# Kernel optimization log

Measured on AMD Instinct MI355X. Metric: run time of the kernel, lower is better.

Reference implementation:

```python
import jax, jax.numpy as jnp
import numpy as np


def setup_inputs() -> dict:
    key = jax.random.key(0)
    D, H, T, B = 512, 512, 500, 128
    ks = jax.random.split(key, 12)
    tn = lambda k, shape: 0.01 * jax.random.truncated_normal(k, -2.0, 2.0, shape, dtype=jnp.float32)
    return {
        "inputs": jax.random.normal(ks[0], (B, D), dtype=jnp.float32),
        "Wz": tn(ks[1], (D, H)),
        "Wr": tn(ks[2], (D, H)),
        "Wh": tn(ks[3], (D, H)),
        "Uz": tn(ks[4], (H, H)),
        "Ur": tn(ks[5], (H, H)),
        "Uh": tn(ks[6], (H, H)),
        "bz": tn(ks[7], (H,)),
        "br": tn(ks[8], (H,)),
        "bh": tn(ks[9], (H,)),
        "Wo": tn(ks[10], (H, D)),
        "bo": tn(ks[11], (D,)),
        "T": T,
    }


def reference(inputs, Wz, Wr, Wh, Uz, Ur, Uh, bz, br, bh, Wo, bo, T):
    B, D = inputs.shape
    H = Wz.shape[1]

    def step(carry, _):
        h, x = carry  # h: [B,H], x: [B,D]
        r = jax.nn.sigmoid(x @ Wr + h @ Ur + br)
        h_prop = jnp.tanh(x @ Wh + (r * h) @ Uh + bh)
        z = jax.nn.sigmoid(x @ Wz + h @ Uz + bz)
        h_new = jnp.clip((1.0 - z) * h + z * h_prop, -5.0, 5.0)
        out = h_new @ Wo + bo
        return (h_new, out), out

    h0 = jnp.zeros((B, H), dtype=inputs.dtype)
    _, outs = jax.lax.scan(step, (h0, inputs), None, length=T - 1)  # [T-1,B,D]
    full = jnp.concatenate([inputs[None], outs], axis=0)  # [T,B,D]
    return jnp.transpose(full, (1, 0, 2))  # [B,T,D]
```

## Files before the change

### kernel.cpp

```cpp
#include <hip/hip_runtime.h>
#include <cstdint>

#define NB 128
#define DH 512
#define ROWS 528

#define OFF_M   0u
#define OFF_M1  1048576u
#define OFF_UH  2097152u
#define OFF_H   2359296u
#define OFF_RH  2426880u
#define OFF_XT  2494464u
#define OFF_GZ  2562048u
#define OFF_GH  2627584u
#define OFF_CV  2693120u
#define OFF_C1  2695168u
#define OFF_BAR 2697216u

__device__ __forceinline__ float sigm(float x) { return 1.f / (1.f + __expf(-x)); }
__device__ __forceinline__ float tanh_fast(float x) {
  float e = __expf(2.f * fminf(x, 40.f));
  return (e - 1.f) / (e + 1.f);
}

__device__ __forceinline__ float cload(const float* p) {
  return __hip_atomic_load(p, __ATOMIC_RELAXED, __HIP_MEMORY_SCOPE_AGENT);
}
__device__ __forceinline__ void cstore(float* p, float v) {
  __hip_atomic_store(p, v, __ATOMIC_RELAXED, __HIP_MEMORY_SCOPE_AGENT);
}

__global__ __launch_bounds__(256) void gru_pre(
    const float* __restrict__ inputs,
    const float* __restrict__ Wz, const float* __restrict__ Wr, const float* __restrict__ Wh,
    const float* __restrict__ Uz, const float* __restrict__ Ur, const float* __restrict__ Uh,
    const float* __restrict__ bz, const float* __restrict__ br, const float* __restrict__ bh,
    const float* __restrict__ Wo, const float* __restrict__ bo,
    float* __restrict__ ws)
{
  __shared__ float sh[8960];
  const int bid = blockIdx.x, t = threadIdx.x;
  float* Mw  = ws + OFF_M;
  float* M1w = ws + OFF_M1;
  float* Uhw = ws + OFF_UH;
  float* hw  = ws + OFF_H;
  float* rhw = ws + OFF_RH;
  float* xT  = ws + OFF_XT;
  float* cv  = ws + OFF_CV;
  float* c1  = ws + OFF_C1;
  uint32_t* bar = (uint32_t*)(ws + OFF_BAR);

  if (bid < 256) {
    const int kh = bid >> 7, cch = bid & 127;
    const int reg = cch >> 5;
    const int k0 = kh * 256, c0 = cch * 16;
    if (reg == 3) {
      const int cc0 = c0 - 1536;
      for (int i = 0; i < 16; ++i) {
        int idx = t + i * 256;
        int kk = k0 + (idx >> 4), ci = idx & 15;
        Mw[(cch * 512 + kk) * 16 + ci] = Wo[kk * 512 + cc0 + ci];
      }
    } else {
      const float* Ws = (reg == 0) ? Wr : (reg == 1) ? Wz : Wh;
      const float* Us = (reg == 0) ? Ur : (reg == 1) ? Uz : nullptr;
      const int cc0 = c0 - reg * 512;
      const int kl = t;
      const int k = k0 + kl;
      float acc[16];
      #pragma unroll
      for (int c = 0; c < 16; ++c) acc[c] = 0.f;
      for (int jt = 0; jt < 16; ++jt) {
        __syncthreads();
        for (int i = 0; i < 32; ++i) {
          int idx = t + i * 256;
          int kk = idx >> 5, jj = idx & 31;
          sh[kk * 35 + jj] = Wo[(k0 + kk) * 512 + jt * 32 + jj];
        }
        __syncthreads();
        for (int j = 0; j < 32; ++j) {
          float wv = sh[kl * 35 + j];
          const float* wrow = Ws + (jt * 32 + j) * 512 + cc0;
          #pragma unroll
          for (int c = 0; c < 16; ++c) acc[c] = fmaf(wv, wrow[c], acc[c]);
        }
      }
      #pragma unroll
      for (int c = 0; c < 16; ++c) {
        float v = acc[c];
        if (Us) v += Us[k * 512 + cc0 + c];
        Mw[(cch * 512 + k) * 16 + c] = v;
      }
    }
  }
  else if (bid < 264) {
    const int q = bid - 256;
    const int r2 = q >> 1;
    const float* Ws = (r2 == 0) ? Wr : (r2 == 1) ? Wz : (r2 == 2) ? Wh : nullptr;
    const float* bs = (r2 == 0) ? br : (r2 == 1) ? bz : (r2 == 2) ? bh : nullptr;
    for (int round = 0; round < 8; ++round) {
      int col32 = t >> 3, strip = t & 7;
      int c = q * 256 + round * 32 + col32;
      int cc = c & 511;
      float p = 0.f;
      if (r2 < 3) {
        for (int j = strip * 64; j < strip * 64 + 64; ++j)
          p = fmaf(bo[j], Ws[j * 512 + cc], p);
      }
      sh[col32 * 8 + strip] = p;
      __syncthreads();
      if (t < 32) {
        float v = 0.f;
        #pragma unroll
        for (int st = 0; st < 8; ++st) v += sh[t * 8 + st];
        int c2 = q * 256 + round * 32 + t;
        int cc2 = c2 & 511;
        cv[c2] = (r2 < 3) ? (v + bs[cc2]) : bo[cc2];
      }
      __syncthreads();
    }
  }
  else if (bid < 288) {
    const int q = bid - 264;
    for (int cq = 0; cq < 4; ++cq) {
      int ch = q * 4 + cq;
      int r3 = ch >> 5;
      const float* Ws = (r3 == 0) ? Wr : (r3 == 1) ? Wz : Wh;
      int cc0 = (ch & 31) * 16;
      for (int i = 0; i < 32; ++i) {
        int idx = t + i * 256;
        int kk = idx >> 4, ci = idx & 15;
        M1w[(ch * 512 + kk) * 16 + ci] = Ws[kk * 512 + cc0 + ci];
      }
    }
  }
  else if (bid < 296) {
    const int q = bid - 288;
    for (int cq = 0; cq < 4; ++cq) {
      int ch = 96 + q * 4 + cq;
      for (int i = 0; i < 32; ++i) {
        int idx = t + i * 256;
        M1w[ch * 8192 + idx] = 0.f;
      }
    }
  }
  else if (bid < 312) {
    const int q = bid - 296;
    for (int cq = 0; cq < 4; ++cq) {
      int ch = q * 4 + cq;
      for (int i = 0; i < 16; ++i) {
        int idx = t + i * 256;
        int kk = idx >> 3, ci = idx & 7;
        Uhw[(ch * 512 + kk) * 8 + ci] = Uh[kk * 512 + ch * 8 + ci];
      }
    }
  }
  else if (bid < 316) {
    const int q = bid - 312;
    for (int ti = q * 4; ti < q * 4 + 4; ++ti) {
      int bt = ti >> 3, dt = ti & 7;
      __syncthreads();
      for (int i = 0; i < 16; ++i) {
        int idx = t + i * 256;
        int r = idx >> 6, c = idx & 63;
        sh[r * 65 + c] = inputs[(bt * 64 + r) * 512 + dt * 64 + c];
      }
      __syncthreads();
      for (int i = 0; i < 16; ++i) {
        int idx = t + i * 256;
        int r = idx >> 6, c = idx & 63;
        xT[(dt * 64 + r) * 128 + bt * 64 + c] = sh[c * 65 + r];
      }
    }
    if (q == 0) {
      for (int idx = t; idx < 16 * 128; idx += 256) xT[512 * 128 + idx] = 0.f;
    }
  }
  else if (bid == 316) {
    for (int idx = t; idx < ROWS * 128; idx += 256) hw[idx] = 0.f;
  }
  else if (bid == 317) {
    for (int idx = t; idx < 16 * 128; idx += 256) rhw[512 * 128 + idx] = 0.f;
  }
  else if (bid == 318) {
    for (int idx = t; idx < 2048; idx += 256)
      c1[idx] = (idx < 512) ? br[idx] : (idx < 1024) ? bz[idx - 512]
              : (idx < 1536) ? bh[idx - 1024] : 0.f;
    for (int idx = t; idx < 1024; idx += 256) bar[idx] = 0u;
  }
}

__device__ __forceinline__ void gbar(uint32_t* bar, int xcd, uint32_t ph) {
  __syncthreads();
  if (threadIdx.x == 0) {
    uint32_t o = __hip_atomic_fetch_add(&bar[xcd * 32], 1u, __ATOMIC_RELAXED, __HIP_MEMORY_SCOPE_AGENT);
    if (o == ph * 32u + 31u) {
      uint32_t g = __hip_atomic_fetch_add(&bar[256], 1u, __ATOMIC_RELAXED, __HIP_MEMORY_SCOPE_AGENT);
      if (g == ph * 8u + 7u) {
        #pragma unroll
        for (int x = 0; x < 8; ++x)
          __hip_atomic_store(&bar[512 + x * 32], ph + 1u, __ATOMIC_RELAXED, __HIP_MEMORY_SCOPE_AGENT);
      }
    }
    int guard = 0;
    while (__hip_atomic_load(&bar[512 + xcd * 32], __ATOMIC_RELAXED, __HIP_MEMORY_SCOPE_AGENT) < ph + 1u) {
      __builtin_amdgcn_s_sleep(1);
      if (++guard > (1 << 22)) break;
    }
  }
  __syncthreads();
}

__global__ __launch_bounds__(512, 2) void gru_main(
    const float* __restrict__ inputs,
    const float* __restrict__ Mw, const float* __restrict__ M1w,
    const float* __restrict__ Uhw,
    const float* __restrict__ cvec, const float* __restrict__ c1vec,
    float* __restrict__ hw, float* __restrict__ rhw,
    const float* __restrict__ xT,
    float* __restrict__ Gz, float* __restrict__ Gh,
    uint32_t* __restrict__ bar, float* __restrict__ out, const int T)
{
  __shared__ float Ald[8192];
  __shared__ float Uld[4096];
  __shared__ float red[4096];
  __shared__ float ttr[1024];

  const int bid = blockIdx.x, tid = threadIdx.x;
  const int wave = __builtin_amdgcn_readfirstlane(tid >> 6);
  const int lane = tid & 63;
  const int bh = bid >> 7, chnk = bid & 127;
  const int typ = chnk >> 5;
  const int b = bh * 64 + lane;
  const int xcd = bid & 7;
  uint32_t ph = 0;

  {
    const float* src = M1w + chnk * 8192;
    #pragma unroll
    for (int i = 0; i < 4; ++i) {
      const int idx4 = tid + i * 512;
      *(float4*)&Ald[idx4 * 4] = *(const float4*)&src[idx4 * 4];
    }
    if (bid < 128) {
      const float* us = Uhw + (size_t)(bid & 63) * 4096;
      *(float4*)&Uld[tid * 4]        = ((const float4*)us)[tid];
      *(float4*)&Uld[2048 + tid * 4] = ((const float4*)us)[512 + tid];
    }
  }
  __syncthreads();

  for (int s = 1; s <= T; ++s) {
    {
      const float* hsrc = (s == 1) ? xT : hw;
      const float* cv = (s == 1) ? c1vec : cvec;
      float acc[16];
      #pragma unroll
      for (int c = 0; c < 16; ++c) acc[c] = 0.f;
      const float* hp = hsrc + (wave * 64) * 128 + b;
      float hv[32];
      #pragma unroll
      for (int u = 0; u < 32; ++u) hv[u] = cload(hp + u * 128);
      #pragma unroll
      for (int u = 0; u < 32; ++u) {
        const float cur = hv[u];
        hv[u] = cload(hp + (32 + u) * 128);
        const float* mrow = &Ald[(wave * 64 + u) * 16];
        #pragma unroll
        for (int c = 0; c < 16; ++c) acc[c] = fmaf(cur, mrow[c], acc[c]);
      }
      #pragma unroll
      for (int u = 0; u < 32; ++u) {
        const float* mrow = &Ald[(wave * 64 + 32 + u) * 16];
        #pragma unroll
        for (int c = 0; c < 16; ++c) acc[c] = fmaf(hv[u], mrow[c], acc[c]);
      }
      if (wave >= 4) {
        #pragma unroll
        for (int c = 0; c < 16; ++c) red[((wave - 4) * 16 + c) * 64 + lane] = acc[c];
      }
      __syncthreads();
      if (wave < 4) {
        #pragma unroll
        for (int c = 0; c < 16; ++c) red[(wave * 16 + c) * 64 + lane] += acc[c];
      }
      __syncthreads();
      const int cg = tid >> 6, lane_ = tid & 63;
      const int bb = bh * 64 + lane_;
      float vout[2];
      #pragma unroll
      for (int i = 0; i < 2; ++i) {
        const int c = cg * 2 + i;
        float v = red[c * 64 + lane_] + red[(16 + c) * 64 + lane_]
                + red[(32 + c) * 64 + lane_] + red[(48 + c) * 64 + lane_];
        vout[i] = v + cv[chnk * 16 + c];
      }
      if (typ == 0) {
        #pragma unroll
        for (int i = 0; i < 2; ++i) {
          const int cglob = chnk * 16 + cg * 2 + i;
          cstore(&rhw[cglob * 128 + bb], sigm(vout[i]) * cload(&hw[cglob * 128 + bb]));
        }
      } else if (typ == 1) {
        #pragma unroll
        for (int i = 0; i < 2; ++i) {
          const int cglob = chnk * 16 + cg * 2 + i;
          cstore(&Gz[(cglob - 512) * 128 + bb], sigm(vout[i]));
        }
      } else if (typ == 2) {
        #pragma unroll
        for (int i = 0; i < 2; ++i) {
          const int cglob = chnk * 16 + cg * 2 + i;
          cstore(&Gh[(cglob - 1024) * 128 + bb], vout[i]);
        }
      } else if (s > 1) {
        #pragma unroll
        for (int i = 0; i < 2; ++i) ttr[lane_ * 16 + cg * 2 + i] = vout[i];
        __syncthreads();
        const int bq = tid >> 3, pr = tid & 7;
        const float2 o2 = *(const float2*)&ttr[bq * 16 + pr * 2];
        const int bglob = bh * 64 + bq;
        const int d0 = (chnk - 96) * 16 + pr * 2;
        *(float2*)&out[(size_t)bglob * (size_t)T * 512 + (size_t)(s - 1) * 512 + d0] = o2;
      }
    }
    gbar(bar, xcd, ph++);

    if (s < T) {
      if (s == 1) {
        const float* src = Mw + chnk * 8192;
        #pragma unroll
        for (int i = 0; i < 4; ++i) {
          const int idx4 = tid + i * 512;
          *(float4*)&Ald[idx4 * 4] = *(const float4*)&src[idx4 * 4];
        }
        if (bid >= 128) {
          const int j = bid - 128;
          for (int idx = tid; idx < 512; idx += 512)
            ;
          if (tid < 512)
            out[(size_t)j * (size_t)T * 512 + tid] = inputs[j * 512 + tid];
        }
      }
      if (bid < 128) {
        const int bh2 = bid >> 6, ch8 = bid & 63;
        const int b2 = bh2 * 64 + lane;
        float acc2[8];
        #pragma unroll
        for (int c = 0; c < 8; ++c) acc2[c] = 0.f;
        const float* rp = rhw + (wave * 64) * 128 + b2;
        float hv[32];
        #pragma unroll
        for (int u = 0; u < 32; ++u) hv[u] = cload(rp + u * 128);
        #pragma unroll
        for (int u = 0; u < 32; ++u) {
          const float cur = hv[u];
          hv[u] = cload(rp + (32 + u) * 128);
          const float* urow = &Uld[(wave * 64 + u) * 8];
          #pragma unroll
          for (int c = 0; c < 8; ++c) acc2[c] = fmaf(cur, urow[c], acc2[c]);
        }
        #pragma unroll
        for (int u = 0; u < 32; ++u) {
          const float* urow = &Uld[(wave * 64 + 32 + u) * 8];
          #pragma unroll
          for (int c = 0; c < 8; ++c) acc2[c] = fmaf(hv[u], urow[c], acc2[c]);
        }
        if (wave >= 4) {
          #pragma unroll
          for (int c = 0; c < 8; ++c) red[((wave - 4) * 8 + c) * 64 + lane] = acc2[c];
        }
        __syncthreads();
        if (wave < 4) {
          #pragma unroll
          for (int c = 0; c < 8; ++c) red[(wave * 8 + c) * 64 + lane] += acc2[c];
        }
        __syncthreads();
        const int cg = tid >> 6, lane_ = tid & 63;
        const float S = red[cg * 64 + lane_] + red[(8 + cg) * 64 + lane_]
                      + red[(16 + cg) * 64 + lane_] + red[(24 + cg) * 64 + lane_];
        const int c = ch8 * 8 + cg;
        const int bb = bh2 * 64 + lane_;
        const float z = cload(&Gz[c * 128 + bb]);
        const float gh = cload(&Gh[c * 128 + bb]) + S;
        const float hprev = cload(&hw[c * 128 + bb]);
        float hn = (1.f - z) * hprev + z * tanh_fast(gh);
        hn = fminf(5.f, fmaxf(-5.f, hn));
        cstore(&hw[c * 128 + bb], hn);
      }
      gbar(bar, xcd, ph++);
    }
  }
}

extern "C" void kernel_launch(void* const* d_in, const int* in_sizes, int n_in,
                              void* d_out, int out_size, void* d_ws, size_t ws_size,
                              hipStream_t stream) {
  const float* inputs = (const float*)d_in[0];
  const float* Wz = (const float*)d_in[1];
  const float* Wr = (const float*)d_in[2];
  const float* Wh = (const float*)d_in[3];
  const float* Uz = (const float*)d_in[4];
  const float* Ur = (const float*)d_in[5];
  const float* Uh = (const float*)d_in[6];
  const float* bz = (const float*)d_in[7];
  const float* br = (const float*)d_in[8];
  const float* bh = (const float*)d_in[9];
  const float* Wo = (const float*)d_in[10];
  const float* bo = (const float*)d_in[11];
  float* ws = (float*)d_ws;
  const int T = out_size / (128 * 512);

  gru_pre<<<dim3(320), dim3(256), 0, stream>>>(inputs, Wz, Wr, Wh, Uz, Ur, Uh,
                                               bz, br, bh, Wo, bo, ws);
  gru_main<<<dim3(256), dim3(512), 0, stream>>>(
      inputs, ws + OFF_M, ws + OFF_M1, ws + OFF_UH, ws + OFF_CV, ws + OFF_C1,
      ws + OFF_H, ws + OFF_RH, ws + OFF_XT, ws + OFF_GZ, ws + OFF_GH,
      (uint32_t*)(ws + OFF_BAR), (float*)d_out, T);
}
```

Before: 7.071 ms.

## Spread Uh phase over all blocks and split grid barrier into arrive/wait

The second per-step phase (r*h @ Uh plus the h update) now runs on all 256 blocks with 4 output columns each, where before 128 blocks handled 8 columns each and the rest sat idle. The Uh staging layout is changed to match. The hierarchical per-XCD barrier becomes a single global counter with split arrive and wait, so the output-projection blocks can write results after arriving and overlap that work with the barrier. The cost is more contention on one atomic counter and each block loading the full rh vector for fewer columns.

```diff
diff --git a/kernel.cpp b/kernel.cpp
--- a/kernel.cpp
+++ b/kernel.cpp
@@ -146,12 +146,12 @@
   }
   else if (bid < 312) {
     const int q = bid - 296;
-    for (int cq = 0; cq < 4; ++cq) {
-      int ch = q * 4 + cq;
-      for (int i = 0; i < 16; ++i) {
-        int idx = t + i * 256;
-        int kk = idx >> 3, ci = idx & 7;
-        Uhw[(ch * 512 + kk) * 8 + ci] = Uh[kk * 512 + ch * 8 + ci];
+    for (int cq = 0; cq < 8; ++cq) {
+      int ch = q * 8 + cq;
+      for (int i = 0; i < 8; ++i) {
+        int idx = t + i * 256;
+        int kk = idx >> 2, ci = idx & 3;
+        Uhw[(ch * 512 + kk) * 4 + ci] = Uh[kk * 512 + ch * 4 + ci];
       }
     }
   }
@@ -186,29 +186,27 @@
     for (int idx = t; idx < 2048; idx += 256)
       c1[idx] = (idx < 512) ? br[idx] : (idx < 1024) ? bz[idx - 512]
               : (idx < 1536) ? bh[idx - 1024] : 0.f;
-    for (int idx = t; idx < 1024; idx += 256) bar[idx] = 0u;
-  }
-}
-
-__device__ __forceinline__ void gbar(uint32_t* bar, int xcd, uint32_t ph) {
+    for (int idx = t; idx < 4096; idx += 256) bar[idx] = 0u;
+  }
+}
+
+__device__ __forceinline__ void gbar_arrive(uint32_t* bar, uint32_t ph) {
   __syncthreads();
   if (threadIdx.x == 0) {
-    uint32_t o = __hip_atomic_fetch_add(&bar[xcd * 32], 1u, __ATOMIC_RELAXED, __HIP_MEMORY_SCOPE_AGENT);
-    if (o == ph * 32u + 31u) {
-      uint32_t g = __hip_atomic_fetch_add(&bar[256], 1u, __ATOMIC_RELAXED, __HIP_MEMORY_SCOPE_AGENT);
-      if (g == ph * 8u + 7u) {
-        #pragma unroll
-        for (int x = 0; x < 8; ++x)
-          __hip_atomic_store(&bar[512 + x * 32], ph + 1u, __ATOMIC_RELAXED, __HIP_MEMORY_SCOPE_AGENT);
-      }
-    }
-    int guard = 0;
-    while (__hip_atomic_load(&bar[512 + xcd * 32], __ATOMIC_RELAXED, __HIP_MEMORY_SCOPE_AGENT) < ph + 1u) {
-      __builtin_amdgcn_s_sleep(1);
-      if (++guard > (1 << 22)) break;
-    }
-  }
-  __syncthreads();
+    uint32_t g = __hip_atomic_fetch_add(&bar[0], 1u, __ATOMIC_RELAXED, __HIP_MEMORY_SCOPE_AGENT);
+    if (g == ph * 256u + 255u) {
+      #pragma unroll
+      for (int x = 0; x < 8; ++x)
+        __hip_atomic_store(&bar[64 + x * 32], ph + 1u, __ATOMIC_RELAXED, __HIP_MEMORY_SCOPE_AGENT);
+    }
+  }
+}
+__device__ __forceinline__ void gbar_wait(uint32_t* bar, int xcls, uint32_t ph) {
+  int guard = 0;
+  while (__hip_atomic_load(&bar[64 + xcls * 32], __ATOMIC_RELAXED, __HIP_MEMORY_SCOPE_AGENT) < ph + 1u) {
+    __builtin_amdgcn_s_sleep(1);
+    if (++guard > (1 << 22)) break;
+  }
 }
 
 __global__ __launch_bounds__(512, 2) void gru_main(
@@ -222,7 +220,7 @@
     uint32_t* __restrict__ bar, float* __restrict__ out, const int T)
 {
   __shared__ float Ald[8192];
-  __shared__ float Uld[4096];
+  __shared__ float Uld[2048];
   __shared__ float red[4096];
   __shared__ float ttr[1024];
 
@@ -232,21 +230,17 @@
   const int bh = bid >> 7, chnk = bid & 127;
   const int typ = chnk >> 5;
   const int b = bh * 64 + lane;
-  const int xcd = bid & 7;
+  const int xcls = bid & 7;
   uint32_t ph = 0;
 
   {
-    const float* src = M1w + chnk * 8192;
+    const float* src = M1w + (size_t)chnk * 8192;
     #pragma unroll
     for (int i = 0; i < 4; ++i) {
       const int idx4 = tid + i * 512;
       *(float4*)&Ald[idx4 * 4] = *(const float4*)&src[idx4 * 4];
     }
-    if (bid < 128) {
-      const float* us = Uhw + (size_t)(bid & 63) * 4096;
-      *(float4*)&Uld[tid * 4]        = ((const float4*)us)[tid];
-      *(float4*)&Uld[2048 + tid * 4] = ((const float4*)us)[512 + tid];
-    }
+    *(float4*)&Uld[tid * 4] = ((const float4*)(Uhw + (size_t)chnk * 2048))[tid];
   }
   __syncthreads();
 
@@ -295,100 +289,108 @@
                 + red[(32 + c) * 64 + lane_] + red[(48 + c) * 64 + lane_];
         vout[i] = v + cv[chnk * 16 + c];
       }
-      if (typ == 0) {
-        #pragma unroll
-        for (int i = 0; i < 2; ++i) {
-          const int cglob = chnk * 16 + cg * 2 + i;
-          cstore(&rhw[cglob * 128 + bb], sigm(vout[i]) * cload(&hw[cglob * 128 + bb]));
-        }
-      } else if (typ == 1) {
-        #pragma unroll
-        for (int i = 0; i < 2; ++i) {
-          const int cglob = chnk * 16 + cg * 2 + i;
-          cstore(&Gz[(cglob - 512) * 128 + bb], sigm(vout[i]));
-        }
-      } else if (typ == 2) {
-        #pragma unroll
-        for (int i = 0; i < 2; ++i) {
-          const int cglob = chnk * 16 + cg * 2 + i;
-          cstore(&Gh[(cglob - 1024) * 128 + bb], vout[i]);
-        }
-      } else if (s > 1) {
-        #pragma unroll
-        for (int i = 0; i < 2; ++i) ttr[lane_ * 16 + cg * 2 + i] = vout[i];
-        __syncthreads();
-        const int bq = tid >> 3, pr = tid & 7;
-        const float2 o2 = *(const float2*)&ttr[bq * 16 + pr * 2];
-        const int bglob = bh * 64 + bq;
-        const int d0 = (chnk - 96) * 16 + pr * 2;
-        *(float2*)&out[(size_t)bglob * (size_t)T * 512 + (size_t)(s - 1) * 512 + d0] = o2;
-      }
-    }
-    gbar(bar, xcd, ph++);
+      if (typ < 3) {
+        if (typ == 0) {
+          #pragma unroll
+          for (int i = 0; i < 2; ++i) {
+            const int cglob = chnk * 16 + cg * 2 + i;
+            cstore(&rhw[cglob * 128 + bb], sigm(vout[i]) * cload(&hw[cglob * 128 + bb]));
+          }
+        } else if (typ == 1) {
+          #pragma unroll
+          for (int i = 0; i < 2; ++i) {
+            const int cglob = chnk * 16 + cg * 2 + i;
+            cstore(&Gz[(cglob - 512) * 128 + bb], sigm(vout[i]));
+          }
+        } else {
+          #pragma unroll
+          for (int i = 0; i < 2; ++i) {
+            const int cglob = chnk * 16 + cg * 2 + i;
+            cstore(&Gh[(cglob - 1024) * 128 + bb], vout[i]);
+          }
+        }
+        gbar_arrive(bar, ph);
+      } else {
+        gbar_arrive(bar, ph);
+        if (s > 1) {
+          #pragma unroll
+          for (int i = 0; i < 2; ++i) ttr[lane_ * 16 + cg * 2 + i] = vout[i];
+          __syncthreads();
+          const int bq = tid >> 3, pr = tid & 7;
+          const float2 o2 = *(const float2*)&ttr[bq * 16 + pr * 2];
+          const int bglob = bh * 64 + bq;
+          const int d0 = (chnk - 96) * 16 + pr * 2;
+          *(float2*)&out[(size_t)bglob * (size_t)T * 512 + (size_t)(s - 1) * 512 + d0] = o2;
+        }
+      }
+    }
+    gbar_wait(bar, xcls, ph); ++ph;
 
     if (s < T) {
       if (s == 1) {
-        const float* src = Mw + chnk * 8192;
+        const float* src = Mw + (size_t)chnk * 8192;
         #pragma unroll
         for (int i = 0; i < 4; ++i) {
           const int idx4 = tid + i * 512;
           *(float4*)&Ald[idx4 * 4] = *(const float4*)&src[idx4 * 4];
         }
-        if (bid >= 128) {
-          const int j = bid - 128;
-          for (int idx = tid; idx < 512; idx += 512)
-            ;
-          if (tid < 512)
-            out[(size_t)j * (size_t)T * 512 + tid] = inputs[j * 512 + tid];
-        }
-      }
-      if (bid < 128) {
-        const int bh2 = bid >> 6, ch8 = bid & 63;
-        const int b2 = bh2 * 64 + lane;
-        float acc2[8];
-        #pragma unroll
-        for (int c = 0; c < 8; ++c) acc2[c] = 0.f;
-        const float* rp = rhw + (wave * 64) * 128 + b2;
+        if (tid < 256) {
+          const int g = bid * 256 + tid;
+          out[(size_t)(g >> 9) * (size_t)T * 512 + (g & 511)] = inputs[g];
+        }
+      }
+      {
+        const int ch4 = chnk;
+        float zf = 0.f, ghf = 0.f, hprev = 0.f;
+        const int c_loc = tid >> 6, bb3 = tid & 63;
+        if (c_loc < 4) {
+          const int cg2 = ch4 * 4 + c_loc;
+          zf    = cload(&Gz[cg2 * 128 + bh * 64 + bb3]);
+          ghf   = cload(&Gh[cg2 * 128 + bh * 64 + bb3]);
+          hprev = cload(&hw[cg2 * 128 + bh * 64 + bb3]);
+        }
+        const float* rp = rhw + (wave * 64) * 128 + b;
         float hv[32];
         #pragma unroll
         for (int u = 0; u < 32; ++u) hv[u] = cload(rp + u * 128);
+        float a2[4];
+        #pragma unroll
+        for (int c = 0; c < 4; ++c) a2[c] = 0.f;
         #pragma unroll
         for (int u = 0; u < 32; ++u) {
           const float cur = hv[u];
           hv[u] = cload(rp + (32 + u) * 128);
-          const float* urow = &Uld[(wave * 64 + u) * 8];
-          #pragma unroll
-          for (int c = 0; c < 8; ++c) acc2[c] = fmaf(cur, urow[c], acc2[c]);
+          const float* urow = &Uld[(wave * 64 + u) * 4];
+          #pragma unroll
+          for (int c = 0; c < 4; ++c) a2[c] = fmaf(cur, urow[c], a2[c]);
         }
         #pragma unroll
         for (int u = 0; u < 32; ++u) {
-          const float* urow = &Uld[(wave * 64 + 32 + u) * 8];
-          #pragma unroll
-          for (int c = 0; c < 8; ++c) acc2[c] = fmaf(hv[u], urow[c], acc2[c]);
+          const float* urow = &Uld[(wave * 64 + 32 + u) * 4];
+          #pragma unroll
+          for (int c = 0; c < 4; ++c) a2[c] = fmaf(hv[u], urow[c], a2[c]);
         }
         if (wave >= 4) {
           #pragma unroll
-          for (int c = 0; c < 8; ++c) red[((wave - 4) * 8 + c) * 64 + lane] = acc2[c];
+          for (int c = 0; c < 4; ++c) red[((wave - 4) * 4 + c) * 64 + lane] = a2[c];
         }
         __syncthreads();
         if (wave < 4) {
           #pragma unroll
-          for (int c = 0; c < 8; ++c) red[(wave * 8 + c) * 64 + lane] += acc2[c];
+          for (int c = 0; c < 4; ++c) red[(wave * 4 + c) * 64 + lane] += a2[c];
         }
         __syncthreads();
-        const int cg = tid >> 6, lane_ = tid & 63;
-        const float S = red[cg * 64 + lane_] + red[(8 + cg) * 64 + lane_]
-                      + red[(16 + cg) * 64 + lane_] + red[(24 + cg) * 64 + lane_];
-        const int c = ch8 * 8 + cg;
-        const int bb = bh2 * 64 + lane_;
-        const float z = cload(&Gz[c * 128 + bb]);
-        const float gh = cload(&Gh[c * 128 + bb]) + S;
-        const float hprev = cload(&hw[c * 128 + bb]);
-        float hn = (1.f - z) * hprev + z * tanh_fast(gh);
-        hn = fminf(5.f, fmaxf(-5.f, hn));
-        cstore(&hw[c * 128 + bb], hn);
-      }
-      gbar(bar, xcd, ph++);
+        if (c_loc < 4) {
+          const float S = red[(c_loc) * 64 + bb3]      + red[(4 + c_loc) * 64 + bb3]
+                        + red[(8 + c_loc) * 64 + bb3]  + red[(12 + c_loc) * 64 + bb3];
+          const int cg2 = ch4 * 4 + c_loc;
+          float hn = (1.f - zf) * hprev + zf * tanh_fast(ghf + S);
+          hn = fminf(5.f, fmaxf(-5.f, hn));
+          cstore(&hw[cg2 * 128 + bh * 64 + bb3], hn);
+        }
+        gbar_arrive(bar, ph);
+      }
+      gbar_wait(bar, xcls, ph); ++ph;
     }
   }
 }
```

Measured after the change: 8.317 ms. 17.6% more time.

## Split grid barrier into producer-specific flags and double-buffer hidden state

Applied to the files above, without the earlier changes.

Replaces the single all-block grid barrier after the gate phase with separate arrive/wait counters for r-gate producers, z/h/out producers, and hidden-state producers. The h-update blocks now wait only for the rh data before their Uh matvec and for the z/h gates just before the final combine, so the Uh matvec can overlap with the remaining gate blocks. The hidden state is double-buffered so that blocks can proceed without a second full barrier racing on overwrites. This adds more barrier counters and a shorter spin guard, and it risks subtle ordering bugs.

```diff
diff --git a/kernel.cpp b/kernel.cpp
--- a/kernel.cpp
+++ b/kernel.cpp
@@ -16,6 +16,7 @@
 #define OFF_CV  2693120u
 #define OFF_C1  2695168u
 #define OFF_BAR 2697216u
+#define OFF_H2  2701312u
 
 __device__ __forceinline__ float sigm(float x) { return 1.f / (1.f + __expf(-x)); }
 __device__ __forceinline__ float tanh_fast(float x) {
@@ -43,7 +44,8 @@
   float* Mw  = ws + OFF_M;
   float* M1w = ws + OFF_M1;
   float* Uhw = ws + OFF_UH;
-  float* hw  = ws + OFF_H;
+  float* hw0 = ws + OFF_H;
+  float* hw1 = ws + OFF_H2;
   float* rhw = ws + OFF_RH;
   float* xT  = ws + OFF_XT;
   float* cv  = ws + OFF_CV;
@@ -177,7 +179,7 @@
     }
   }
   else if (bid == 316) {
-    for (int idx = t; idx < ROWS * 128; idx += 256) hw[idx] = 0.f;
+    for (int idx = t; idx < ROWS * 128; idx += 256) hw0[idx] = 0.f;
   }
   else if (bid == 317) {
     for (int idx = t; idx < 16 * 128; idx += 256) rhw[512 * 128 + idx] = 0.f;
@@ -186,26 +188,42 @@
     for (int idx = t; idx < 2048; idx += 256)
       c1[idx] = (idx < 512) ? br[idx] : (idx < 1024) ? bz[idx - 512]
               : (idx < 1536) ? bh[idx - 1024] : 0.f;
-    for (int idx = t; idx < 1024; idx += 256) bar[idx] = 0u;
-  }
-}
-
-__device__ __forceinline__ void gbar(uint32_t* bar, int xcd, uint32_t ph) {
+    for (int idx = t; idx < 4096; idx += 256) bar[idx] = 0u;
+  }
+  else if (bid == 319) {
+    for (int idx = t; idx < ROWS * 128; idx += 256) hw1[idx] = 0.f;
+  }
+}
+
+#define BAR_R 0
+#define BAR_G 1024
+#define BAR_B 2048
+
+__device__ __forceinline__ void arrive(uint32_t* bar, int base, int xcls,
+                                       uint32_t perCls, uint32_t ph) {
   __syncthreads();
   if (threadIdx.x == 0) {
-    uint32_t o = __hip_atomic_fetch_add(&bar[xcd * 32], 1u, __ATOMIC_RELAXED, __HIP_MEMORY_SCOPE_AGENT);
-    if (o == ph * 32u + 31u) {
-      uint32_t g = __hip_atomic_fetch_add(&bar[256], 1u, __ATOMIC_RELAXED, __HIP_MEMORY_SCOPE_AGENT);
+    uint32_t o = __hip_atomic_fetch_add(&bar[base + xcls * 32], 1u,
+                                        __ATOMIC_RELAXED, __HIP_MEMORY_SCOPE_AGENT);
+    if (o == ph * perCls + (perCls - 1u)) {
+      uint32_t g = __hip_atomic_fetch_add(&bar[base + 256], 1u,
+                                          __ATOMIC_RELAXED, __HIP_MEMORY_SCOPE_AGENT);
       if (g == ph * 8u + 7u) {
         #pragma unroll
         for (int x = 0; x < 8; ++x)
-          __hip_atomic_store(&bar[512 + x * 32], ph + 1u, __ATOMIC_RELAXED, __HIP_MEMORY_SCOPE_AGENT);
-      }
-    }
+          __hip_atomic_store(&bar[base + 512 + x * 32], ph + 1u,
+                             __ATOMIC_RELAXED, __HIP_MEMORY_SCOPE_AGENT);
+      }
+    }
+  }
+}
+__device__ __forceinline__ void waitf(uint32_t* bar, int base, int xcls, uint32_t ph) {
+  if (threadIdx.x == 0) {
     int guard = 0;
-    while (__hip_atomic_load(&bar[512 + xcd * 32], __ATOMIC_RELAXED, __HIP_MEMORY_SCOPE_AGENT) < ph + 1u) {
+    while (__hip_atomic_load(&bar[base + 512 + xcls * 32],
+                             __ATOMIC_RELAXED, __HIP_MEMORY_SCOPE_AGENT) < ph + 1u) {
       __builtin_amdgcn_s_sleep(1);
-      if (++guard > (1 << 22)) break;
+      if (++guard > (1 << 18)) break;
     }
   }
   __syncthreads();
@@ -216,7 +234,8 @@
     const float* __restrict__ Mw, const float* __restrict__ M1w,
     const float* __restrict__ Uhw,
     const float* __restrict__ cvec, const float* __restrict__ c1vec,
-    float* __restrict__ hw, float* __restrict__ rhw,
+    float* __restrict__ hw0, float* __restrict__ hw1,
+    float* __restrict__ rhw,
     const float* __restrict__ xT,
     float* __restrict__ Gz, float* __restrict__ Gh,
     uint32_t* __restrict__ bar, float* __restrict__ out, const int T)
@@ -232,18 +251,20 @@
   const int bh = bid >> 7, chnk = bid & 127;
   const int typ = chnk >> 5;
   const int b = bh * 64 + lane;
-  const int xcd = bid & 7;
-  uint32_t ph = 0;
+  const int xcls = bid & 7;
+  const bool isB = (bid < 128);
+  const int bh2 = bid >> 6, ch8 = bid & 63;
+  const int cg = tid >> 6, lane_ = tid & 63;
 
   {
-    const float* src = M1w + chnk * 8192;
+    const float* src = M1w + (size_t)chnk * 8192;
     #pragma unroll
     for (int i = 0; i < 4; ++i) {
       const int idx4 = tid + i * 512;
       *(float4*)&Ald[idx4 * 4] = *(const float4*)&src[idx4 * 4];
     }
-    if (bid < 128) {
-      const float* us = Uhw + (size_t)(bid & 63) * 4096;
+    if (isB) {
+      const float* us = Uhw + (size_t)ch8 * 4096;
       *(float4*)&Uld[tid * 4]        = ((const float4*)us)[tid];
       *(float4*)&Uld[2048 + tid * 4] = ((const float4*)us)[512 + tid];
     }
@@ -251,9 +272,20 @@
   __syncthreads();
 
   for (int s = 1; s <= T; ++s) {
+    const int p = s & 1;
+    const float* hcur = p ? hw1 : hw0;
+    float* hnxt = p ? hw0 : hw1;
+    const uint32_t ph = (uint32_t)(s - 1);
+
     {
-      const float* hsrc = (s == 1) ? xT : hw;
+      const float* hsrc = (s == 1) ? xT : hcur;
       const float* cv = (s == 1) ? c1vec : cvec;
+      float hpre[2];
+      if (typ == 0) {
+        #pragma unroll
+        for (int i = 0; i < 2; ++i)
+          hpre[i] = cload(&hcur[(chnk * 16 + cg * 2 + i) * 128 + bh * 64 + lane_]);
+      }
       float acc[16];
       #pragma unroll
       for (int c = 0; c < 16; ++c) acc[c] = 0.f;
@@ -285,7 +317,6 @@
         for (int c = 0; c < 16; ++c) red[(wave * 16 + c) * 64 + lane] += acc[c];
       }
       __syncthreads();
-      const int cg = tid >> 6, lane_ = tid & 63;
       const int bb = bh * 64 + lane_;
       float vout[2];
       #pragma unroll
@@ -299,96 +330,99 @@
         #pragma unroll
         for (int i = 0; i < 2; ++i) {
           const int cglob = chnk * 16 + cg * 2 + i;
-          cstore(&rhw[cglob * 128 + bb], sigm(vout[i]) * cload(&hw[cglob * 128 + bb]));
-        }
+          cstore(&rhw[cglob * 128 + bb], sigm(vout[i]) * hpre[i]);
+        }
+        if (s < T) arrive(bar, BAR_R, xcls, 8, ph);
       } else if (typ == 1) {
         #pragma unroll
         for (int i = 0; i < 2; ++i) {
           const int cglob = chnk * 16 + cg * 2 + i;
           cstore(&Gz[(cglob - 512) * 128 + bb], sigm(vout[i]));
         }
+        if (s < T) arrive(bar, BAR_G, xcls, 24, ph);
       } else if (typ == 2) {
         #pragma unroll
         for (int i = 0; i < 2; ++i) {
           const int cglob = chnk * 16 + cg * 2 + i;
           cstore(&Gh[(cglob - 1024) * 128 + bb], vout[i]);
         }
-      } else if (s > 1) {
-        #pragma unroll
-        for (int i = 0; i < 2; ++i) ttr[lane_ * 16 + cg * 2 + i] = vout[i];
-        __syncthreads();
-        const int bq = tid >> 3, pr = tid & 7;
-        const float2 o2 = *(const float2*)&ttr[bq * 16 + pr * 2];
-        const int bglob = bh * 64 + bq;
-        const int d0 = (chnk - 96) * 16 + pr * 2;
-        *(float2*)&out[(size_t)bglob * (size_t)T * 512 + (size_t)(s - 1) * 512 + d0] = o2;
-      }
-    }
-    gbar(bar, xcd, ph++);
+        if (s < T) arrive(bar, BAR_G, xcls, 24, ph);
+      } else {
+        if (s < T) arrive(bar, BAR_G, xcls, 24, ph);
+        if (s > 1) {
+          #pragma unroll
+          for (int i = 0; i < 2; ++i) ttr[lane_ * 16 + cg * 2 + i] = vout[i];
+          __syncthreads();
+          const int bq = tid >> 3, pr = tid & 7;
+          const float2 o2 = *(const float2*)&ttr[bq * 16 + pr * 2];
+          const int bglob = bh * 64 + bq;
+          const int d0 = (chnk - 96) * 16 + pr * 2;
+          *(float2*)&out[(size_t)bglob * (size_t)T * 512 + (size_t)(s - 1) * 512 + d0] = o2;
+        }
+      }
+    }
+
+    if (s == 1) {
+      __syncthreads();
+      const float* src = Mw + (size_t)chnk * 8192;
+      #pragma unroll
+      for (int i = 0; i < 4; ++i) {
+        const int idx4 = tid + i * 512;
+        *(float4*)&Ald[idx4 * 4] = *(const float4*)&src[idx4 * 4];
+      }
+      if (tid < 256) {
+        const int g = bid * 256 + tid;
+        out[(size_t)(g >> 9) * (size_t)T * 512 + (g & 511)] = inputs[g];
+      }
+    }
 
     if (s < T) {
-      if (s == 1) {
-        const float* src = Mw + chnk * 8192;
-        #pragma unroll
-        for (int i = 0; i < 4; ++i) {
-          const int idx4 = tid + i * 512;
-          *(float4*)&Ald[idx4 * 4] = *(const float4*)&src[idx4 * 4];
-        }
-        if (bid >= 128) {
-          const int j = bid - 128;
-          for (int idx = tid; idx < 512; idx += 512)
-            ;
-          if (tid < 512)
-            out[(size_t)j * (size_t)T * 512 + tid] = inputs[j * 512 + tid];
-        }
-      }
-      if (bid < 128) {
-        const int bh2 = bid >> 6, ch8 = bid & 63;
-        const int b2 = bh2 * 64 + lane;
-        float acc2[8];
-        #pragma unroll
-        for (int c = 0; c < 8; ++c) acc2[c] = 0.f;
-        const float* rp = rhw + (wave * 64) * 128 + b2;
+      if (isB) {
+        waitf(bar, BAR_R, xcls, ph);
+        const int cg2 = ch8 * 8 + cg;
+        const int bb2 = bh2 * 64 + lane_;
+        const float hprev = cload(&hcur[cg2 * 128 + bb2]);
+        const float* rp = rhw + (wave * 64) * 128 + bh2 * 64 + lane;
         float hv[32];
         #pragma unroll
         for (int u = 0; u < 32; ++u) hv[u] = cload(rp + u * 128);
+        float a2[8];
+        #pragma unroll
+        for (int c = 0; c < 8; ++c) a2[c] = 0.f;
         #pragma unroll
         for (int u = 0; u < 32; ++u) {
           const float cur = hv[u];
           hv[u] = cload(rp + (32 + u) * 128);
           const float* urow = &Uld[(wave * 64 + u) * 8];
           #pragma unroll
-          for (int c = 0; c < 8; ++c) acc2[c] = fmaf(cur, urow[c], acc2[c]);
+          for (int c = 0; c < 8; ++c) a2[c] = fmaf(cur, urow[c], a2[c]);
         }
         #pragma unroll
         for (int u = 0; u < 32; ++u) {
           const float* urow = &Uld[(wave * 64 + 32 + u) * 8];
           #pragma unroll
-          for (int c = 0; c < 8; ++c) acc2[c] = fmaf(hv[u], urow[c], acc2[c]);
+          for (int c = 0; c < 8; ++c) a2[c] = fmaf(hv[u], urow[c], a2[c]);
         }
         if (wave >= 4) {
           #pragma unroll
-          for (int c = 0; c < 8; ++c) red[((wave - 4) * 8 + c) * 64 + lane] = acc2[c];
+          for (int c = 0; c < 8; ++c) red[((wave - 4) * 8 + c) * 64 + lane] = a2[c];
         }
         __syncthreads();
         if (wave < 4) {
           #pragma unroll
-          for (int c = 0; c < 8; ++c) red[(wave * 8 + c) * 64 + lane] += acc2[c];
-        }
-        __syncthreads();
-        const int cg = tid >> 6, lane_ = tid & 63;
+          for (int c = 0; c < 8; ++c) red[(wave * 8 + c) * 64 + lane] += a2[c];
+        }
+        waitf(bar, BAR_G, xcls, ph);
+        const float zf  = cload(&Gz[cg2 * 128 + bb2]);
+        const float ghf = cload(&Gh[cg2 * 128 + bb2]);
         const float S = red[cg * 64 + lane_] + red[(8 + cg) * 64 + lane_]
                       + red[(16 + cg) * 64 + lane_] + red[(24 + cg) * 64 + lane_];
-        const int c = ch8 * 8 + cg;
-        const int bb = bh2 * 64 + lane_;
-        const float z = cload(&Gz[c * 128 + bb]);
-        const float gh = cload(&Gh[c * 128 + bb]) + S;
-        const float hprev = cload(&hw[c * 128 + bb]);
-        float hn = (1.f - z) * hprev + z * tanh_fast(gh);
+        float hn = (1.f - zf) * hprev + zf * tanh_fast(ghf + S);
         hn = fminf(5.f, fmaxf(-5.f, hn));
-        cstore(&hw[c * 128 + bb], hn);
-      }
-      gbar(bar, xcd, ph++);
+        cstore(&hnxt[cg2 * 128 + bb2], hn);
+        arrive(bar, BAR_B, xcls, 16, ph);
+      }
+      waitf(bar, BAR_B, xcls, ph);
     }
   }
 }
@@ -415,6 +449,6 @@
                                                bz, br, bh, Wo, bo, ws);
   gru_main<<<dim3(256), dim3(512), 0, stream>>>(
       inputs, ws + OFF_M, ws + OFF_M1, ws + OFF_UH, ws + OFF_CV, ws + OFF_C1,
-      ws + OFF_H, ws + OFF_RH, ws + OFF_XT, ws + OFF_GZ, ws + OFF_GH,
+      ws + OFF_H, ws + OFF_H2, ws + OFF_RH, ws + OFF_XT, ws + OFF_GZ, ws + OFF_GH,
       (uint32_t*)(ws + OFF_BAR), (float*)d_out, T);
 }
```

Result: no change. 6.969 ms (-1.4%).
